# Kernel optimization log

Hardware: AMD Instinct MI355X
Metric: run time of the kernel (lower is better)

The kernel has to match this reference:

```python
import jax, jax.numpy as jnp
import numpy as np

FACTOR = 5

def setup_inputs() -> dict:
    key = jax.random.key(0)
    k1, k2, k3, k4 = jax.random.split(key, 4)
    B, L, H, D = 4, 2048, 8, 64
    sample_k = min(FACTOR * int(np.ceil(np.log(L))), L)  # 40
    return {
        "queries": jax.random.normal(k1, (B, L, H, D), dtype=jnp.float32),
        "keys": jax.random.normal(k2, (B, L, H, D), dtype=jnp.float32),
        "values": jax.random.normal(k3, (B, L, H, D), dtype=jnp.float32),
        "index_sample": jax.random.randint(k4, (L, sample_k), 0, L, dtype=jnp.int32),
    }

def reference(queries, keys, values, index_sample):
    # [B, L, H, D] -> [B, H, L, D]
    Q = jnp.transpose(queries, (0, 2, 1, 3))
    K = jnp.transpose(keys, (0, 2, 1, 3))
    V = jnp.transpose(values, (0, 2, 1, 3))
    B, H, L_Q, D = Q.shape
    L_K = K.shape[2]
    u = min(FACTOR * int(np.ceil(np.log(L_Q))), L_Q)  # n_top

    # --- _prob_QK: sampled QK scores ---
    # K_sample: [B, H, L_Q, sample_k, D]
    K_sample = K[:, :, index_sample, :]
    # Q_K_sample[b,h,l,s] = Q[b,h,l,:] . K_sample[b,h,l,s,:]
    Q_K_sample = jnp.einsum('bhld,bhlsd->bhls', Q, K_sample)
    # sparsity measure M: max - mean over L_K
    M = Q_K_sample.max(axis=-1) - Q_K_sample.sum(axis=-1) / L_K  # [B,H,L_Q]
    _, M_top = jax.lax.top_k(M, u)  # [B,H,u]

    # reduced Q -> full scores against all keys
    Q_reduce = jnp.take_along_axis(Q, M_top[..., None], axis=2)  # [B,H,u,D]
    scores = jnp.einsum('bhud,bhkd->bhuk', Q_reduce, K)  # [B,H,u,L_K]
    scale = 1.0 / jnp.sqrt(jnp.asarray(D, dtype=scores.dtype))
    scores = scores * scale

    # --- initial context: mean of V over keys (mask_flag=False) ---
    V_mean = V.mean(axis=-2)  # [B,H,D]
    context = jnp.broadcast_to(V_mean[:, :, None, :], (B, H, L_Q, D))

    # --- update context at top-u query positions ---
    attn = jax.nn.softmax(scores, axis=-1)  # [B,H,u,L_K]
    ctx_top = jnp.einsum('bhuk,bhkd->bhud', attn, V)  # [B,H,u,D]
    b_idx = jnp.arange(B)[:, None, None]
    h_idx = jnp.arange(H)[None, :, None]
    context = context.at[b_idx, h_idx, M_top].set(ctx_top)
    return context  # [B, H, L_Q, D]
```

## Files before the change

kernel.cpp:

```cpp
#include <hip/hip_runtime.h>
#include <math.h>

#define LL 2048
#define HH 8
#define DD 64
#define SK 40
#define UU 40
#define SCALE 0.125f


__global__ __launch_bounds__(512, 4) void k_m(
    const float* __restrict__ Q, const float* __restrict__ K,
    const int* __restrict__ idxs, float* __restrict__ Mout)
{
  __shared__ int sidx[8 * SK];
  int bx = blockIdx.x;
  int xcd = bx & 7, slot = bx >> 3;
  int b = xcd >> 1;
  int l0 = ((xcd & 1) << 10) | (slot << 3);
  int t = threadIdx.x;
  int w = t >> 6, lane = t & 63;
  int l = l0 + w;
  int h = lane >> 3, dg = lane & 7;

  if (t < 8 * SK) sidx[t] = idxs[l0 * SK + t];

  const float4* Q4 = (const float4*)Q;
  int qoff = (((b << 11) + l) << 7) + (h << 4) + (dg << 1);
  float4 q0 = Q4[qoff], q1 = Q4[qoff + 1];

  const float4* K4 = (const float4*)K;
  int kbb = b << 18;
  int klo = (h << 4) + (dg << 1);

  __syncthreads();

  float mx = -INFINITY, sum = 0.f;
#pragma unroll
  for (int s0 = 0; s0 < SK; s0 += 8) {
    float4 ka[8], kc[8];
#pragma unroll
    for (int j = 0; j < 8; ++j) {
      int idx = sidx[w * SK + s0 + j];
      int off = kbb + (idx << 7) + klo;
      ka[j] = K4[off];
      kc[j] = K4[off + 1];
    }
#pragma unroll
    for (int j = 0; j < 8; ++j) {
      float p = q0.x * ka[j].x + q0.y * ka[j].y + q0.z * ka[j].z + q0.w * ka[j].w
              + q1.x * kc[j].x + q1.y * kc[j].y + q1.z * kc[j].z + q1.w * kc[j].w;
      p += __shfl_xor(p, 1);
      p += __shfl_xor(p, 2);
      p += __shfl_xor(p, 4);
      mx = fmaxf(mx, p);
      sum += p;
    }
  }
  if (dg == 0) Mout[((b * HH + h) << 11) + l] = mx - sum * (1.0f / (float)LL);
}

__global__ __launch_bounds__(256) void k_topk(
    const float* __restrict__ Mv, int* __restrict__ Mtop)
{
  __shared__ float sv[LL];
  __shared__ float wm[4];
  __shared__ int wi[4];
  int bh = blockIdx.x;
  int t = threadIdx.x, w = t >> 6, ln = t & 63;
  for (int i = t; i < LL; i += 256) sv[i] = Mv[bh * LL + i];
  __syncthreads();
  for (int r = 0; r < UU; ++r) {
    float bv = -INFINITY; int bi = 0;
#pragma unroll
    for (int j = 0; j < 8; ++j) {
      int i = t + (j << 8);
      float v = sv[i];
      if (v > bv) { bv = v; bi = i; }
    }
#pragma unroll
    for (int off = 1; off < 64; off <<= 1) {
      float ov = __shfl_xor(bv, off);
      int oi = __shfl_xor(bi, off);
      if (ov > bv || (ov == bv && oi < bi)) { bv = ov; bi = oi; }
    }
    if (ln == 0) { wm[w] = bv; wi[w] = bi; }
    __syncthreads();
    if (t == 0) {
      float Bv = wm[0]; int Bi = wi[0];
#pragma unroll
      for (int k = 1; k < 4; ++k)
        if (wm[k] > Bv || (wm[k] == Bv && wi[k] < Bi)) { Bv = wm[k]; Bi = wi[k]; }
      Mtop[bh * UU + r] = Bi;
      sv[Bi] = -INFINITY;
    }
    __syncthreads();
  }
}

__global__ __launch_bounds__(256) void k_vpart(
    const float* __restrict__ V, float* __restrict__ part)
{
  int blk = blockIdx.x;
  int bh = blk >> 3, c = blk & 7;
  int b = bh >> 3, h = bh & 7;
  int t = threadIdx.x, d = t & 63, w = t >> 6;
  int l0 = (c << 8) + (w << 6);
  int base = (b << 20) + (l0 << 9) + (h << 6) + d;
  float a0 = 0, a1 = 0, a2 = 0, a3 = 0;
  for (int j = 0; j < 64; j += 4) {
    a0 += V[base + ((j + 0) << 9)];
    a1 += V[base + ((j + 1) << 9)];
    a2 += V[base + ((j + 2) << 9)];
    a3 += V[base + ((j + 3) << 9)];
  }
  __shared__ float sm[4][64];
  sm[w][d] = a0 + a1 + a2 + a3;
  __syncthreads();
  if (t < 64) part[(blk << 6) + t] = sm[0][t] + sm[1][t] + sm[2][t] + sm[3][t];
}

__global__ __launch_bounds__(256) void k_fill(
    const float4* __restrict__ part4, float4* __restrict__ out4)
{
  int i = blockIdx.x * 256 + threadIdx.x;
  int bh = i >> 15;
  __shared__ float4 vm[16];
  if (threadIdx.x < 16) {
    int d4 = threadIdx.x;
    float4 s = {0, 0, 0, 0};
#pragma unroll
    for (int c = 0; c < 8; ++c) {
      float4 p = part4[((bh << 3) + c) * 16 + d4];
      s.x += p.x; s.y += p.y; s.z += p.z; s.w += p.w;
    }
    const float inv = 1.0f / (float)LL;
    s.x *= inv; s.y *= inv; s.z *= inv; s.w *= inv;
    vm[d4] = s;
  }
  __syncthreads();
  out4[i] = vm[i & 15];
}

__global__ __launch_bounds__(512) void k_attn2(
    const float* __restrict__ Q, const float* __restrict__ K,
    const float* __restrict__ V, const int* __restrict__ Mtop,
    float* __restrict__ pm, float* __restrict__ pl, float4* __restrict__ pO4)
{
  __shared__ float4 Ks4[1024];
  __shared__ float Ps[8][256];
  __shared__ float4 Os4[4][2][4][16];
  __shared__ int gqi[8];

  int bx = blockIdx.x;
  int ch = bx & 7;
  int slot = bx >> 3;
  int bh = slot / 5, rg = slot % 5;
  int b = bh >> 3, h = bh & 7;
  int t = threadIdx.x;
  int w = t >> 6, ln = t & 63;
  int l0 = ch << 8;

  if (t < 8) gqi[t] = Mtop[bh * UU + rg * 8 + t];
  __syncthreads();

  float4 qv[16];
  {
    const float4* qrow = (const float4*)Q + (((b << 11) + gqi[w]) << 7) + (h << 4);
#pragma unroll
    for (int i = 0; i < 16; ++i) qv[i] = qrow[i];
  }

  const float4* K4 = (const float4*)K;
  int kbase = (((b << 11) + l0) << 7) + (h << 4);
  int col0 = t >> 4, d40 = t & 15;
  int sw0 = col0 * 16 + (d40 ^ (col0 & 7));
  float4 g0 = K4[kbase + col0 * 128 + d40];
  float4 g1 = K4[kbase + (col0 + 32) * 128 + d40];

  float sc[4];
#pragma unroll
  for (int st = 0; st < 4; ++st) {
    __syncthreads();
    Ks4[sw0] = g0;
    Ks4[sw0 + 512] = g1;
    float4 n0, n1;
    if (st < 3) {
      int lr = (st + 1) * 64;
      n0 = K4[kbase + (lr + col0) * 128 + d40];
      n1 = K4[kbase + (lr + col0 + 32) * 128 + d40];
    }
    __syncthreads();
    float s = 0.f;
#pragma unroll
    for (int d4 = 0; d4 < 16; ++d4) {
      float4 kv = Ks4[ln * 16 + (d4 ^ (ln & 7))];
      s += qv[d4].x * kv.x + qv[d4].y * kv.y + qv[d4].z * kv.z + qv[d4].w * kv.w;
    }
    sc[st] = s * SCALE;
    g0 = n0; g1 = n1;
  }

  float m = fmaxf(fmaxf(sc[0], sc[1]), fmaxf(sc[2], sc[3]));
#pragma unroll
  for (int off = 1; off < 64; off <<= 1) m = fmaxf(m, __shfl_xor(m, off));
  float lsum = 0.f;
#pragma unroll
  for (int st = 0; st < 4; ++st) {
    float p = __expf(sc[st] - m);
    Ps[w][st * 64 + ln] = p;
    lsum += p;
  }
#pragma unroll
  for (int off = 1; off < 64; off <<= 1) lsum += __shfl_xor(lsum, off);
  if (ln == 0) {
    int prow = bh * UU + rg * 8 + w;
    pm[prow * 8 + ch] = m;
    pl[prow * 8 + ch] = lsum;
  }
  __syncthreads();

  int rw = w >> 2, cq = w & 3;
  int cg = ln >> 4, d4 = ln & 15;
  float4 o0 = {0,0,0,0}, o1 = {0,0,0,0}, o2 = {0,0,0,0}, o3 = {0,0,0,0};
  int vb = (((b << 11) + l0 + cq * 64) << 7) + (h << 4);
  const float4* V4 = (const float4*)V;
#pragma unroll
  for (int i = 0; i < 16; ++i) {
    int c = i * 4 + cg;
    float4 v4 = V4[vb + c * 128 + d4];
    float p0 = Ps[rw * 4 + 0][cq * 64 + c];
    float p1 = Ps[rw * 4 + 1][cq * 64 + c];
    float p2 = Ps[rw * 4 + 2][cq * 64 + c];
    float p3 = Ps[rw * 4 + 3][cq * 64 + c];
    o0.x += p0 * v4.x; o0.y += p0 * v4.y; o0.z += p0 * v4.z; o0.w += p0 * v4.w;
    o1.x += p1 * v4.x; o1.y += p1 * v4.y; o1.z += p1 * v4.z; o1.w += p1 * v4.w;
    o2.x += p2 * v4.x; o2.y += p2 * v4.y; o2.z += p2 * v4.z; o2.w += p2 * v4.w;
    o3.x += p3 * v4.x; o3.y += p3 * v4.y; o3.z += p3 * v4.z; o3.w += p3 * v4.w;
  }
#pragma unroll
  for (int off = 16; off <= 32; off <<= 1) {
    o0.x += __shfl_xor(o0.x, off); o0.y += __shfl_xor(o0.y, off);
    o0.z += __shfl_xor(o0.z, off); o0.w += __shfl_xor(o0.w, off);
    o1.x += __shfl_xor(o1.x, off); o1.y += __shfl_xor(o1.y, off);
    o1.z += __shfl_xor(o1.z, off); o1.w += __shfl_xor(o1.w, off);
    o2.x += __shfl_xor(o2.x, off); o2.y += __shfl_xor(o2.y, off);
    o2.z += __shfl_xor(o2.z, off); o2.w += __shfl_xor(o2.w, off);
    o3.x += __shfl_xor(o3.x, off); o3.y += __shfl_xor(o3.y, off);
    o3.z += __shfl_xor(o3.z, off); o3.w += __shfl_xor(o3.w, off);
  }
  if (cg == 0) {
    Os4[cq][rw][0][d4] = o0;
    Os4[cq][rw][1][d4] = o1;
    Os4[cq][rw][2][d4] = o2;
    Os4[cq][rw][3][d4] = o3;
  }
  __syncthreads();

  if (t < 128) {
    int r = t >> 4, dd = t & 15;
    float4 a = Os4[0][r >> 2][r & 3][dd];
    float4 bq = Os4[1][r >> 2][r & 3][dd];
    float4 cc = Os4[2][r >> 2][r & 3][dd];
    float4 dq = Os4[3][r >> 2][r & 3][dd];
    float4 s;
    s.x = a.x + bq.x + cc.x + dq.x;
    s.y = a.y + bq.y + cc.y + dq.y;
    s.z = a.z + bq.z + cc.z + dq.z;
    s.w = a.w + bq.w + cc.w + dq.w;
    int prow = bh * UU + rg * 8 + r;
    pO4[(prow * 8 + ch) * 16 + dd] = s;
  }
}

__global__ __launch_bounds__(256) void k_comb(
    const float* __restrict__ pm, const float* __restrict__ pl,
    const float* __restrict__ pO, const int* __restrict__ Mtop,
    float* __restrict__ out)
{
  int row = blockIdx.x * 4 + (threadIdx.x >> 6);
  int ln = threadIdx.x & 63;
  int bh = row / UU, r40 = row % UU;
  float mm[8];
#pragma unroll
  for (int c = 0; c < 8; ++c) mm[c] = pm[row * 8 + c];
  float ms = mm[0];
#pragma unroll
  for (int c = 1; c < 8; ++c) ms = fmaxf(ms, mm[c]);
  float wsum = 0.f, o = 0.f;
#pragma unroll
  for (int c = 0; c < 8; ++c) {
    float wc = __expf(mm[c] - ms);
    wsum += wc * pl[row * 8 + c];
    o += wc * pO[(row * 8 + c) * 64 + ln];
  }
  int gq = Mtop[bh * UU + r40];
  out[((bh * LL + gq) << 6) + ln] = o / wsum;
}

extern "C" void kernel_launch(void* const* d_in, const int* in_sizes, int n_in,
                              void* d_out, int out_size, void* d_ws, size_t ws_size,
                              hipStream_t stream)
{
  (void)in_sizes; (void)n_in; (void)out_size; (void)ws_size;
  const float* Q = (const float*)d_in[0];
  const float* K = (const float*)d_in[1];
  const float* V = (const float*)d_in[2];
  const int* idxs = (const int*)d_in[3];
  float* out = (float*)d_out;

  float* wsf = (float*)d_ws;
  float* M     = wsf;
  float* part  = wsf + 65536;
  int*   Mtop  = (int*)(wsf + 83968);
  float* pm    = wsf + 85248;
  float* pl    = wsf + 95488;
  float* pO    = wsf + 105728;

  k_m    <<<1024, 512, 0, stream>>>(Q, K, idxs, M);
  k_topk <<<32,   256, 0, stream>>>(M, Mtop);
  k_vpart<<<256,  256, 0, stream>>>(V, part);
  k_fill <<<4096, 256, 0, stream>>>((const float4*)part, (float4*)out);
  k_attn2<<<1280, 512, 0, stream>>>(Q, K, V, Mtop, pm, pl, (float4*)pO);
  k_comb <<<320,  256, 0, stream>>>(pm, pl, pO, Mtop, out);
}
```

Before: 208.0 us.

## Merge M-score and V-mean kernels, merge top-k and fill kernels, remap M lanes

Fuses the sampled-score kernel with the V partial-sum kernel into one launch, split by block index, and fuses the top-k selection with the context fill kernel the same way. This cuts the launch count from six to four, and lets the independent streaming work overlap with the compute-bound parts. The sampled QK kernel now processes 4 query rows per block instead of 8. Each wave handles half the samples for one row, with 4 lanes per head reading strided float4s, and the two halves are combined through shared memory. The costs are extra shared-memory reductions and divergent block roles inside a single kernel.

```diff
diff --git a/kernel.cpp b/kernel.cpp
--- a/kernel.cpp
+++ b/kernel.cpp
@@ -8,138 +8,159 @@
 #define UU 40
 #define SCALE 0.125f
 
-
-__global__ __launch_bounds__(512, 4) void k_m(
+__device__ __forceinline__ float dot4(float4 a, float4 b) {
+  return a.x * b.x + a.y * b.y + a.z * b.z + a.w * b.w;
+}
+
+
+__global__ __launch_bounds__(512, 4) void k_A(
     const float* __restrict__ Q, const float* __restrict__ K,
-    const int* __restrict__ idxs, float* __restrict__ Mout)
-{
-  __shared__ int sidx[8 * SK];
+    const float* __restrict__ V, const int* __restrict__ idxs,
+    float* __restrict__ Mout, float* __restrict__ part)
+{
   int bx = blockIdx.x;
-  int xcd = bx & 7, slot = bx >> 3;
-  int b = xcd >> 1;
-  int l0 = ((xcd & 1) << 10) | (slot << 3);
   int t = threadIdx.x;
-  int w = t >> 6, lane = t & 63;
-  int l = l0 + w;
-  int h = lane >> 3, dg = lane & 7;
-
-  if (t < 8 * SK) sidx[t] = idxs[l0 * SK + t];
-
-  const float4* Q4 = (const float4*)Q;
-  int qoff = (((b << 11) + l) << 7) + (h << 4) + (dg << 1);
-  float4 q0 = Q4[qoff], q1 = Q4[qoff + 1];
-
-  const float4* K4 = (const float4*)K;
-  int kbb = b << 18;
-  int klo = (h << 4) + (dg << 1);
-
-  __syncthreads();
-
-  float mx = -INFINITY, sum = 0.f;
-#pragma unroll
-  for (int s0 = 0; s0 < SK; s0 += 8) {
-    float4 ka[8], kc[8];
-#pragma unroll
-    for (int j = 0; j < 8; ++j) {
-      int idx = sidx[w * SK + s0 + j];
-      int off = kbb + (idx << 7) + klo;
-      ka[j] = K4[off];
-      kc[j] = K4[off + 1];
-    }
-#pragma unroll
-    for (int j = 0; j < 8; ++j) {
-      float p = q0.x * ka[j].x + q0.y * ka[j].y + q0.z * ka[j].z + q0.w * ka[j].w
-              + q1.x * kc[j].x + q1.y * kc[j].y + q1.z * kc[j].z + q1.w * kc[j].w;
-      p += __shfl_xor(p, 1);
-      p += __shfl_xor(p, 2);
-      p += __shfl_xor(p, 4);
-      mx = fmaxf(mx, p);
-      sum += p;
-    }
-  }
-  if (dg == 0) Mout[((b * HH + h) << 11) + l] = mx - sum * (1.0f / (float)LL);
-}
-
-__global__ __launch_bounds__(256) void k_topk(
-    const float* __restrict__ Mv, int* __restrict__ Mtop)
-{
-  __shared__ float sv[LL];
-  __shared__ float wm[4];
-  __shared__ int wi[4];
-  int bh = blockIdx.x;
-  int t = threadIdx.x, w = t >> 6, ln = t & 63;
-  for (int i = t; i < LL; i += 256) sv[i] = Mv[bh * LL + i];
-  __syncthreads();
-  for (int r = 0; r < UU; ++r) {
-    float bv = -INFINITY; int bi = 0;
-#pragma unroll
-    for (int j = 0; j < 8; ++j) {
-      int i = t + (j << 8);
-      float v = sv[i];
-      if (v > bv) { bv = v; bi = i; }
-    }
-#pragma unroll
-    for (int off = 1; off < 64; off <<= 1) {
-      float ov = __shfl_xor(bv, off);
-      int oi = __shfl_xor(bi, off);
-      if (ov > bv || (ov == bv && oi < bi)) { bv = ov; bi = oi; }
-    }
-    if (ln == 0) { wm[w] = bv; wi[w] = bi; }
-    __syncthreads();
-    if (t == 0) {
-      float Bv = wm[0]; int Bi = wi[0];
-#pragma unroll
-      for (int k = 1; k < 4; ++k)
-        if (wm[k] > Bv || (wm[k] == Bv && wi[k] < Bi)) { Bv = wm[k]; Bi = wi[k]; }
-      Mtop[bh * UU + r] = Bi;
-      sv[Bi] = -INFINITY;
-    }
-    __syncthreads();
-  }
-}
-
-__global__ __launch_bounds__(256) void k_vpart(
-    const float* __restrict__ V, float* __restrict__ part)
-{
-  int blk = blockIdx.x;
-  int bh = blk >> 3, c = blk & 7;
-  int b = bh >> 3, h = bh & 7;
-  int t = threadIdx.x, d = t & 63, w = t >> 6;
-  int l0 = (c << 8) + (w << 6);
-  int base = (b << 20) + (l0 << 9) + (h << 6) + d;
-  float a0 = 0, a1 = 0, a2 = 0, a3 = 0;
-  for (int j = 0; j < 64; j += 4) {
-    a0 += V[base + ((j + 0) << 9)];
-    a1 += V[base + ((j + 1) << 9)];
-    a2 += V[base + ((j + 2) << 9)];
-    a3 += V[base + ((j + 3) << 9)];
-  }
-  __shared__ float sm[4][64];
-  sm[w][d] = a0 + a1 + a2 + a3;
-  __syncthreads();
-  if (t < 64) part[(blk << 6) + t] = sm[0][t] + sm[1][t] + sm[2][t] + sm[3][t];
-}
-
-__global__ __launch_bounds__(256) void k_fill(
+
+  if (bx < 2048) {
+    __shared__ int sidx[4 * SK];
+    __shared__ float wred[2][4][2][8];
+
+    int xcd = bx & 7, slot = bx >> 3;
+    int b = xcd >> 1;
+    int l0 = ((xcd & 1) << 10) | (slot << 2);
+    int w = t >> 6, lane = t & 63;
+    int lpos = w >> 1, half = w & 1;
+    int l = l0 + lpos;
+    int h = (lane >> 2) & 7, dg = lane & 3, sp = lane >> 5;
+
+    if (t < 4 * SK) sidx[t] = idxs[l0 * SK + t];
+
+    const float4* Q4 = (const float4*)Q;
+    int qb = (((b << 11) + l) << 7) + (h << 4) + dg;
+    float4 q0 = Q4[qb], q1 = Q4[qb + 4], q2 = Q4[qb + 8], q3 = Q4[qb + 12];
+
+    const float4* K4 = (const float4*)K;
+    int kbb = (b << 18) + (h << 4) + dg;
+
+    __syncthreads();
+
+    const int* hidx = &sidx[lpos * SK + half * 20];
+    float mx = -INFINITY, sum = 0.f;
+#pragma unroll
+    for (int pp = 0; pp < 10; pp += 2) {
+      int i0 = hidx[pp * 2 + sp];
+      int i1 = hidx[pp * 2 + 2 + sp];
+      int o0 = kbb + (i0 << 7);
+      int o1 = kbb + (i1 << 7);
+      float4 a0 = K4[o0], a1 = K4[o0 + 4], a2 = K4[o0 + 8], a3 = K4[o0 + 12];
+      float4 c0 = K4[o1], c1 = K4[o1 + 4], c2 = K4[o1 + 8], c3 = K4[o1 + 12];
+      float p = dot4(q0, a0) + dot4(q1, a1) + dot4(q2, a2) + dot4(q3, a3);
+      float r = dot4(q0, c0) + dot4(q1, c1) + dot4(q2, c2) + dot4(q3, c3);
+      p += __shfl_xor(p, 1); p += __shfl_xor(p, 2);
+      r += __shfl_xor(r, 1); r += __shfl_xor(r, 2);
+      mx = fmaxf(mx, fmaxf(p, r));
+      sum += p + r;
+    }
+    mx = fmaxf(mx, __shfl_xor(mx, 32));
+    sum += __shfl_xor(sum, 32);
+    if ((lane & 35) == 0) {
+      wred[0][lpos][half][h] = mx;
+      wred[1][lpos][half][h] = sum;
+    }
+    __syncthreads();
+    if (t < 32) {
+      int lp = t >> 3, hh = t & 7;
+      float M0 = fmaxf(wred[0][lp][0][hh], wred[0][lp][1][hh]);
+      float S0 = wred[1][lp][0][hh] + wred[1][lp][1][hh];
+      Mout[((b * HH + hh) << 11) + (l0 + lp)] = M0 - S0 * (1.0f / (float)LL);
+    }
+  } else {
+    __shared__ float sm[8][64];
+    int blk = bx - 2048;
+    int bh = blk >> 3, c = blk & 7;
+    int b = bh >> 3, h = bh & 7;
+    int w = t >> 6, d = t & 63;
+    int l0 = (c << 8) + (w << 5);
+    int base = (b << 20) + (l0 << 9) + (h << 6) + d;
+    float a0 = 0, a1 = 0, a2 = 0, a3 = 0;
+#pragma unroll
+    for (int j = 0; j < 32; j += 4) {
+      a0 += V[base + ((j + 0) << 9)];
+      a1 += V[base + ((j + 1) << 9)];
+      a2 += V[base + ((j + 2) << 9)];
+      a3 += V[base + ((j + 3) << 9)];
+    }
+    sm[w][d] = a0 + a1 + a2 + a3;
+    __syncthreads();
+    if (t < 64) {
+      float s = 0;
+#pragma unroll
+      for (int i = 0; i < 8; ++i) s += sm[i][t];
+      part[(blk << 6) + t] = s;
+    }
+  }
+}
+
+__global__ __launch_bounds__(256) void k_B(
+    const float* __restrict__ Mv, int* __restrict__ Mtop,
     const float4* __restrict__ part4, float4* __restrict__ out4)
 {
-  int i = blockIdx.x * 256 + threadIdx.x;
-  int bh = i >> 15;
-  __shared__ float4 vm[16];
-  if (threadIdx.x < 16) {
-    int d4 = threadIdx.x;
-    float4 s = {0, 0, 0, 0};
-#pragma unroll
-    for (int c = 0; c < 8; ++c) {
-      float4 p = part4[((bh << 3) + c) * 16 + d4];
-      s.x += p.x; s.y += p.y; s.z += p.z; s.w += p.w;
-    }
-    const float inv = 1.0f / (float)LL;
-    s.x *= inv; s.y *= inv; s.z *= inv; s.w *= inv;
-    vm[d4] = s;
-  }
-  __syncthreads();
-  out4[i] = vm[i & 15];
+  int bx = blockIdx.x;
+  int t = threadIdx.x;
+
+  if (bx < 32) {
+    __shared__ float sv[LL];
+    __shared__ float wm[4];
+    __shared__ int wi[4];
+    int bh = bx;
+    int w = t >> 6, ln = t & 63;
+    for (int i = t; i < LL; i += 256) sv[i] = Mv[bh * LL + i];
+    __syncthreads();
+    for (int r = 0; r < UU; ++r) {
+      float bv = -INFINITY; int bi = 0;
+#pragma unroll
+      for (int j = 0; j < 8; ++j) {
+        int i = t + (j << 8);
+        float v = sv[i];
+        if (v > bv) { bv = v; bi = i; }
+      }
+#pragma unroll
+      for (int off = 1; off < 64; off <<= 1) {
+        float ov = __shfl_xor(bv, off);
+        int oi = __shfl_xor(bi, off);
+        if (ov > bv || (ov == bv && oi < bi)) { bv = ov; bi = oi; }
+      }
+      if (ln == 0) { wm[w] = bv; wi[w] = bi; }
+      __syncthreads();
+      if (t == 0) {
+        float Bv = wm[0]; int Bi = wi[0];
+#pragma unroll
+        for (int k = 1; k < 4; ++k)
+          if (wm[k] > Bv || (wm[k] == Bv && wi[k] < Bi)) { Bv = wm[k]; Bi = wi[k]; }
+        Mtop[bh * UU + r] = Bi;
+        sv[Bi] = -INFINITY;
+      }
+      __syncthreads();
+    }
+  } else {
+    __shared__ float4 vm[16];
+    int i = (bx - 32) * 256 + t;
+    int bh = i >> 15;
+    if (t < 16) {
+      int d4 = t;
+      float4 s = {0, 0, 0, 0};
+#pragma unroll
+      for (int c = 0; c < 8; ++c) {
+        float4 p = part4[((bh << 3) + c) * 16 + d4];
+        s.x += p.x; s.y += p.y; s.z += p.z; s.w += p.w;
+      }
+      const float inv = 1.0f / (float)LL;
+      s.x *= inv; s.y *= inv; s.z *= inv; s.w *= inv;
+      vm[d4] = s;
+    }
+    __syncthreads();
+    out4[i] = vm[i & 15];
+  }
 }
 
 __global__ __launch_bounds__(512) void k_attn2(
@@ -317,10 +338,8 @@
   float* pl    = wsf + 95488;
   float* pO    = wsf + 105728;
 
-  k_m    <<<1024, 512, 0, stream>>>(Q, K, idxs, M);
-  k_topk <<<32,   256, 0, stream>>>(M, Mtop);
-  k_vpart<<<256,  256, 0, stream>>>(V, part);
-  k_fill <<<4096, 256, 0, stream>>>((const float4*)part, (float4*)out);
+  k_A    <<<2304, 512, 0, stream>>>(Q, K, V, idxs, M, part);
+  k_B    <<<4128, 256, 0, stream>>>(M, Mtop, (const float4*)part, (float4*)out);
   k_attn2<<<1280, 512, 0, stream>>>(Q, K, V, Mtop, pm, pl, (float4*)pO);
   k_comb <<<320,  256, 0, stream>>>(pm, pl, pO, Mtop, out);
 }
```

Measured after the change: 202.7 us. -2.5%, faster.
